# Optimization experiments

Measured on AMD Instinct MI355X. Metric: run time of the kernel, lower is better.

Reference implementation:

```python
import jax, jax.numpy as jnp
import numpy as np

BATCH = 2048
IN_DIM = 512          # group input dim
HID = 1024            # meta_output_dim = dim*2
E = 16                # meta_experts_num = num_experts*2
RANK = 2              # lora_rank
EPS = 1e-5


def setup_inputs() -> dict:
    key = jax.random.key(0)
    ks = jax.random.split(key, 8)
    x = jax.random.normal(ks[0], (BATCH, IN_DIM), jnp.float32)
    gate_states = jax.random.normal(ks[1], (BATCH, IN_DIM), jnp.float32)
    expert_indices = jnp.arange(E, dtype=jnp.int64)
    expert_weights = jax.random.normal(ks[2], (E, IN_DIM, HID), jnp.float32) * 0.02
    expert_biases = jnp.zeros((E, HID), jnp.float32)
    bn_weights = jnp.ones((E, HID), jnp.float32)
    bn_biases = jnp.zeros((E, HID), jnp.float32)
    running_mean = jax.random.normal(ks[3], (E, HID), jnp.float32) * 0.1
    running_var = jnp.abs(jax.random.normal(ks[4], (E, HID), jnp.float32)) * 0.5 + 0.5
    gate_weights = jax.random.normal(ks[5], (IN_DIM, E), jnp.float32) * 0.02
    lora_A = jax.random.normal(ks[6], (IN_DIM, RANK), jnp.float32) * 0.02
    lora_B = jax.random.normal(ks[7], (RANK, IN_DIM), jnp.float32) * 0.02
    return dict(x=x, gate_states=gate_states, expert_indices=expert_indices,
                expert_weights=expert_weights, expert_biases=expert_biases,
                bn_weights=bn_weights, bn_biases=bn_biases,
                running_mean=running_mean, running_var=running_var,
                gate_weights=gate_weights, lora_A=lora_A, lora_B=lora_B)


def reference(x, gate_states, expert_indices, expert_weights, expert_biases,
              bn_weights, bn_biases, running_mean, running_var,
              gate_weights, lora_A, lora_B):
    # LoRA feature gate (lora_gate_forward with sigmoid): x * sigmoid(x A B)
    xg = x * jax.nn.sigmoid((x @ lora_A) @ lora_B)          # [B, D]

    # Expert dispatch: gather selected expert params (home_expert_forward)
    W = expert_weights[expert_indices]                        # [E, D, H]
    b = expert_biases[expert_indices]                         # [E, H]
    h = jnp.einsum('bd,edh->ebh', xg, W) + b[:, None, :]      # [E, B, H]

    # Fused inference BatchNorm + SiLU (fused_batch_norm_silu_forward)
    inv = jax.lax.rsqrt(running_var[expert_indices] + EPS)    # [E, H]
    scale = bn_weights[expert_indices] * inv                  # [E, H]
    shift = bn_biases[expert_indices] - running_mean[expert_indices] * scale
    h = h * scale[:, None, :] + shift[:, None, :]
    h = h * jax.nn.sigmoid(h)                                 # SiLU

    # Softmax gate (gate_weights_forward) and weighted combine
    g = jax.nn.softmax(gate_states @ gate_weights, axis=-1)   # [B, E]
    out = jnp.einsum('ebh,be->bh', h, g)                      # [B, H]
    return out
```

## Files before the change

### kernel.cpp

```cpp
#include <hip/hip_runtime.h>
#include <hip/hip_bf16.h>

#define BATCH 2048
#define IN_DIM 512
#define HID 1024
#define NE 16
#define EPSV 1e-5f

typedef __bf16 bf16x8 __attribute__((ext_vector_type(8)));
typedef float floatx4 __attribute__((ext_vector_type(4)));
typedef unsigned short ushort8 __attribute__((ext_vector_type(8)));

__device__ __forceinline__ unsigned short f2bf(float f) {
  unsigned int u = __builtin_bit_cast(unsigned int, f);
  u += 0x7FFFu + ((u >> 16) & 1u);
  return (unsigned short)(u >> 16);
}

__device__ __forceinline__ int get_expert(const int* __restrict__ idx, int e) {
  bool is64 = (idx[1] == 0) && (idx[3] == 0);
  return is64 ? (int)((const long long*)idx)[e] : idx[e];
}

__device__ __forceinline__ void gld16(void* lds, const void* g) {
  __builtin_amdgcn_global_load_lds(
      (const __attribute__((address_space(1))) void*)g,
      (__attribute__((address_space(3))) void*)lds, 16, 0, 0);
}

__global__ __launch_bounds__(256) void prep_all(
    const int* __restrict__ idx, const float* __restrict__ W,
    unsigned short* __restrict__ WT,
    const float* __restrict__ x, const float* __restrict__ gs,
    const float* __restrict__ gw, const float* __restrict__ lA,
    const float* __restrict__ lB,
    unsigned short* __restrict__ xg, float* __restrict__ g,
    const float* __restrict__ bnw, const float* __restrict__ bnb,
    const float* __restrict__ rmean, const float* __restrict__ rvar,
    const float* __restrict__ ebias,
    float* __restrict__ Ac, float* __restrict__ Cc) {
  int bid = blockIdx.x;
  if (bid < 2048) {
    int e = bid >> 7, kt = (bid >> 4) & 7, ht = bid & 15;
    int ie = get_expert(idx, e);
    int k0 = kt * 64, h0 = ht * 64;
    __shared__ float tile[64][65];
    const float* Wp = W + (size_t)ie * IN_DIM * HID;
#pragma unroll
    for (int i = 0; i < 4; ++i) {
      int id = threadIdx.x + i * 256;
      int k = id >> 4, c = (id & 15) * 4;
      float4 v = *(const float4*)(Wp + (size_t)(k0 + k) * HID + h0 + c);
      tile[k][c] = v.x; tile[k][c + 1] = v.y; tile[k][c + 2] = v.z; tile[k][c + 3] = v.w;
    }
    __syncthreads();
#pragma unroll
    for (int i = 0; i < 2; ++i) {
      int id = threadIdx.x + i * 256;
      int h = id >> 3, kc = (id & 7) * 8;
      ushort8 o;
#pragma unroll
      for (int j = 0; j < 8; ++j) o[j] = f2bf(tile[kc + j][h]);
      *(ushort8*)(WT + ((size_t)e * HID + h0 + h) * IN_DIM + k0 + kc) = o;
    }
  } else if (bid < 2560) {
    int lane = threadIdx.x & 63;
    int b = (bid - 2048) * 4 + (threadIdx.x >> 6);
    const float* xrow = x + (size_t)b * IN_DIM;
    const float* grow = gs + (size_t)b * IN_DIM;
    int d0 = lane * 8;
    float4 xa = *(const float4*)(xrow + d0);
    float4 xb = *(const float4*)(xrow + d0 + 4);
    float xv[8] = {xa.x, xa.y, xa.z, xa.w, xb.x, xb.y, xb.z, xb.w};
    float4 ga = *(const float4*)(grow + d0);
    float4 gb = *(const float4*)(grow + d0 + 4);
    float gv[8] = {ga.x, ga.y, ga.z, ga.w, gb.x, gb.y, gb.z, gb.w};

    float u0 = 0.f, u1 = 0.f;
#pragma unroll
    for (int j = 0; j < 8; ++j) {
      float2 a2 = *(const float2*)(lA + (size_t)(d0 + j) * 2);
      u0 += xv[j] * a2.x;
      u1 += xv[j] * a2.y;
    }
#pragma unroll
    for (int off = 1; off < 64; off <<= 1) {
      u0 += __shfl_xor(u0, off);
      u1 += __shfl_xor(u1, off);
    }
    float ge[16];
#pragma unroll
    for (int e = 0; e < 16; ++e) ge[e] = 0.f;
#pragma unroll
    for (int j = 0; j < 8; ++j) {
      float q = gv[j];
      const float4* gwr = (const float4*)(gw + (size_t)(d0 + j) * NE);
      float4 w0 = gwr[0], w1 = gwr[1], w2 = gwr[2], w3 = gwr[3];
      ge[0] += q * w0.x; ge[1] += q * w0.y; ge[2] += q * w0.z; ge[3] += q * w0.w;
      ge[4] += q * w1.x; ge[5] += q * w1.y; ge[6] += q * w1.z; ge[7] += q * w1.w;
      ge[8] += q * w2.x; ge[9] += q * w2.y; ge[10] += q * w2.z; ge[11] += q * w2.w;
      ge[12] += q * w3.x; ge[13] += q * w3.y; ge[14] += q * w3.z; ge[15] += q * w3.w;
    }
#pragma unroll
    for (int off = 1; off < 64; off <<= 1) {
#pragma unroll
      for (int e = 0; e < 16; ++e) ge[e] += __shfl_xor(ge[e], off);
    }
    float m = ge[0];
#pragma unroll
    for (int e = 1; e < 16; ++e) m = fmaxf(m, ge[e]);
    float p[16], s = 0.f;
#pragma unroll
    for (int e = 0; e < 16; ++e) { p[e] = __expf(ge[e] - m); s += p[e]; }
    float inv = 1.f / s;
    if (lane == 0) {
      float* gout = g + (size_t)b * NE;
#pragma unroll
      for (int e = 0; e < 16; ++e) gout[e] = p[e] * inv;
    }
    ushort8 ov;
#pragma unroll
    for (int j = 0; j < 8; ++j) {
      float t = u0 * lB[d0 + j] + u1 * lB[IN_DIM + d0 + j];
      float sg = __builtin_amdgcn_rcpf(1.f + __expf(-t));
      ov[j] = f2bf(xv[j] * sg);
    }
    *(ushort8*)(xg + (size_t)b * IN_DIM + d0) = ov;
  } else {
    int t = (bid - 2560) * 256 + threadIdx.x;
    int e = t >> 10, h = t & 1023;
    int ie = get_expert(idx, e);
    size_t o = (size_t)ie * HID + h;
    float scale = bnw[o] * rsqrtf(rvar[o] + EPSV);
    Ac[t] = scale;
    Cc[t] = (ebias[o] - rmean[o]) * scale + bnb[o];
  }
}

__global__ __launch_bounds__(256) void zero_out(float* __restrict__ out) {
  int t = blockIdx.x * 256 + threadIdx.x;
  ((float4*)out)[t] = float4{0.f, 0.f, 0.f, 0.f};
}

__global__ __launch_bounds__(256) void reduce4(const float* __restrict__ sws,
                                               float* __restrict__ out) {
  int t = blockIdx.x * 256 + threadIdx.x;
  const float4* s0 = (const float4*)sws;
  const float4* s1 = s0 + (BATCH * HID / 4);
  const float4* s2 = s1 + (BATCH * HID / 4);
  const float4* s3 = s2 + (BATCH * HID / 4);
  float4 a = s0[t], b = s1[t], c = s2[t], d = s3[t];
  ((float4*)out)[t] = float4{a.x + b.x + c.x + d.x, a.y + b.y + c.y + d.y,
                             a.z + b.z + c.z + d.z, a.w + b.w + c.w + d.w};
}

#define BM 128
#define BN 128
#define KS 32
#define EPB 4
#define ESTRIDE ((size_t)HID * IN_DIM)

__global__ __launch_bounds__(256, 2) void moe_main(
    const unsigned short* __restrict__ xg, const unsigned short* __restrict__ WT,
    const float* __restrict__ g, const float* __restrict__ Ac,
    const float* __restrict__ Cc, float* __restrict__ splitws,
    float* __restrict__ out, int use_split) {
  __shared__ __align__(16) unsigned short As[2][2][BM * KS];
  __shared__ __align__(16) unsigned short Bs[2][2][BN * KS];
  __shared__ float gS[BM][EPB];

  int tid = threadIdx.x;
  int lane = tid & 63, w = tid >> 6;
  int wr = w >> 1, wc = w & 1;
  int l15 = lane & 15, quad = lane >> 4;

  int bid = blockIdx.x;
  int p = bid >> 7;
  int rowb = (bid >> 3) & 15, colb = bid & 7;
  int row0 = rowb * BM, col0 = colb * BN;
  int e0 = p * EPB;

  for (int i = tid; i < BM * EPB; i += 256) {
    int r = i >> 2, e = i & 3;
    gS[r][e] = g[(size_t)(row0 + r) * NE + e0 + e];
  }

  int dr = lane >> 2, dk = (lane & 3) * 8;
  const unsigned short* gA = xg + (size_t)(row0 + w * 32 + dr) * IN_DIM + dk;
  const unsigned short* gB0 =
      WT + ((size_t)e0 * HID + col0 + w * 32 + dr) * IN_DIM + dk;

  auto dma = [&](const unsigned short* a, const unsigned short* b, int buf) {
#pragma unroll
    for (int kk = 0; kk < 2; ++kk) {
#pragma unroll
      for (int j = 0; j < 2; ++j) {
        gld16(&As[buf][kk][(w * 32 + j * 16) * KS], a + kk * KS + (size_t)j * 16 * IN_DIM);
        gld16(&Bs[buf][kk][(w * 32 + j * 16) * KS], b + kk * KS + (size_t)j * 16 * IN_DIM);
      }
    }
  };

  floatx4 acc[4][4], oacc[4][4];
#pragma unroll
  for (int rt = 0; rt < 4; ++rt)
#pragma unroll
    for (int ct = 0; ct < 4; ++ct)
#pragma unroll
      for (int r = 0; r < 4; ++r) { acc[rt][ct][r] = 0.f; oacc[rt][ct][r] = 0.f; }

  const unsigned short* gBe = gB0;
  dma(gA, gBe, 0);
  __syncthreads();

  for (int e = 0; e < EPB; ++e) {
    float Acoef[4], Ccoef[4];
#pragma unroll
    for (int ct = 0; ct < 4; ++ct) {
      int colg = col0 + wc * 64 + ct * 16 + l15;
      Acoef[ct] = Ac[(e0 + e) * HID + colg];
      Ccoef[ct] = Cc[(e0 + e) * HID + colg];
    }
#pragma unroll
    for (int s = 0; s < 8; ++s) {
      const int buf = s & 1;
      if (e < EPB - 1 || s < 7) {
        const unsigned short* an = gA + ((s + 1) & 7) * 64;
        const unsigned short* bn = (s < 7) ? (gBe + (s + 1) * 64) : (gBe + ESTRIDE);
        dma(an, bn, buf ^ 1);
      }
#pragma unroll
      for (int kk = 0; kk < 2; ++kk) {
        bf16x8 af[4], bfv[4];
#pragma unroll
        for (int rt = 0; rt < 4; ++rt)
          af[rt] = *(const bf16x8*)&As[buf][kk][(wr * 64 + rt * 16 + l15) * KS + quad * 8];
#pragma unroll
        for (int ct = 0; ct < 4; ++ct)
          bfv[ct] = *(const bf16x8*)&Bs[buf][kk][(wc * 64 + ct * 16 + l15) * KS + quad * 8];
#pragma unroll
        for (int rt = 0; rt < 4; ++rt)
#pragma unroll
          for (int ct = 0; ct < 4; ++ct)
            acc[rt][ct] = __builtin_amdgcn_mfma_f32_16x16x32_bf16(af[rt], bfv[ct], acc[rt][ct], 0, 0, 0);
      }
      if (s == 7) {
#pragma unroll
        for (int ct = 0; ct < 4; ++ct) {
#pragma unroll
          for (int rt = 0; rt < 4; ++rt) {
            int rb = wr * 64 + rt * 16 + quad * 4;
#pragma unroll
            for (int r = 0; r < 4; ++r) {
              float gvw = gS[rb + r][e];
              float z = Acoef[ct] * acc[rt][ct][r] + Ccoef[ct];
              float sg = __builtin_amdgcn_rcpf(1.f + __expf(-z));
              oacc[rt][ct][r] += gvw * z * sg;
              acc[rt][ct][r] = 0.f;
            }
          }
        }
      }
      __syncthreads();
    }
    gBe += ESTRIDE;
  }

  if (use_split) {
    float* sout = splitws + (size_t)p * BATCH * HID;
#pragma unroll
    for (int rt = 0; rt < 4; ++rt)
#pragma unroll
      for (int ct = 0; ct < 4; ++ct)
#pragma unroll
        for (int r = 0; r < 4; ++r)
          sout[(size_t)(row0 + wr * 64 + rt * 16 + quad * 4 + r) * HID +
               col0 + wc * 64 + ct * 16 + l15] = oacc[rt][ct][r];
  } else {
#pragma unroll
    for (int rt = 0; rt < 4; ++rt)
#pragma unroll
      for (int ct = 0; ct < 4; ++ct)
#pragma unroll
        for (int r = 0; r < 4; ++r)
          atomicAdd(&out[(size_t)(row0 + wr * 64 + rt * 16 + quad * 4 + r) * HID +
                         col0 + wc * 64 + ct * 16 + l15], oacc[rt][ct][r]);
  }
}

extern "C" void kernel_launch(void* const* d_in, const int* in_sizes, int n_in,
                              void* d_out, int out_size, void* d_ws, size_t ws_size,
                              hipStream_t stream) {
  const float* x     = (const float*)d_in[0];
  const float* gs    = (const float*)d_in[1];
  const int*   idx   = (const int*)d_in[2];
  const float* W     = (const float*)d_in[3];
  const float* ebias = (const float*)d_in[4];
  const float* bnw   = (const float*)d_in[5];
  const float* bnb   = (const float*)d_in[6];
  const float* rmean = (const float*)d_in[7];
  const float* rvar  = (const float*)d_in[8];
  const float* gw    = (const float*)d_in[9];
  const float* lA    = (const float*)d_in[10];
  const float* lB    = (const float*)d_in[11];
  float* out = (float*)d_out;

  char* ws = (char*)d_ws;
  unsigned short* WT = (unsigned short*)ws;
  unsigned short* xg = (unsigned short*)(ws + 16777216);
  float* g    = (float*)(ws + 18874368);
  float* Acf  = (float*)(ws + 19005440);
  float* Ccf  = (float*)(ws + 19070976);
  float* sws  = (float*)(ws + 19136512);
  int use_split = (ws_size >= 19136512 + 4ull * BATCH * HID * 4) ? 1 : 0;

  prep_all<<<dim3(2624), dim3(256), 0, stream>>>(
      idx, W, WT, x, gs, gw, lA, lB, xg, g, bnw, bnb, rmean, rvar, ebias, Acf, Ccf);
  if (!use_split)
    zero_out<<<dim3(BATCH * HID / 1024), dim3(256), 0, stream>>>(out);
  moe_main<<<dim3((BATCH / BM) * (HID / BN) * (NE / EPB)), dim3(256), 0, stream>>>(
      xg, WT, g, Acf, Ccf, sws, out, use_split);
  if (use_split)
    reduce4<<<dim3(BATCH * HID / 1024), dim3(256), 0, stream>>>(sws, out);
}
```

Measured before the change: 180.6 us.

## Drop split-K workspace reduction, fold output zeroing into prep, hoist LDS fragment loads

Removes the four-way split workspace path and its separate reduce kernel. moe_main now always accumulates into the output with atomicAdd, and zeroing of the output moves into extra blocks of the prep kernel, saving a launch and the extra workspace traffic. The main loop also loads both k-halves of the A/B fragments from LDS before issuing the next DMA, so LDS reads can overlap the prefetch. The cost is contention from four-way float atomics on every output element, a summation order that is no longer deterministic, and higher register pressure from the doubled fragment arrays.

```diff
diff --git a/kernel.cpp b/kernel.cpp
--- a/kernel.cpp
+++ b/kernel.cpp
@@ -38,7 +38,8 @@
     const float* __restrict__ bnw, const float* __restrict__ bnb,
     const float* __restrict__ rmean, const float* __restrict__ rvar,
     const float* __restrict__ ebias,
-    float* __restrict__ Ac, float* __restrict__ Cc) {
+    float* __restrict__ Ac, float* __restrict__ Cc,
+    float* __restrict__ out) {
   int bid = blockIdx.x;
   if (bid < 2048) {
     int e = bid >> 7, kt = (bid >> 4) & 7, ht = bid & 15;
@@ -126,7 +127,7 @@
       ov[j] = f2bf(xv[j] * sg);
     }
     *(ushort8*)(xg + (size_t)b * IN_DIM + d0) = ov;
-  } else {
+  } else if (bid < 2624) {
     int t = (bid - 2560) * 256 + threadIdx.x;
     int e = t >> 10, h = t & 1023;
     int ie = get_expert(idx, e);
@@ -134,24 +135,10 @@
     float scale = bnw[o] * rsqrtf(rvar[o] + EPSV);
     Ac[t] = scale;
     Cc[t] = (ebias[o] - rmean[o]) * scale + bnb[o];
+  } else {
+    int t = (bid - 2624) * 256 + threadIdx.x;
+    ((float4*)out)[t] = float4{0.f, 0.f, 0.f, 0.f};
   }
-}
-
-__global__ __launch_bounds__(256) void zero_out(float* __restrict__ out) {
-  int t = blockIdx.x * 256 + threadIdx.x;
-  ((float4*)out)[t] = float4{0.f, 0.f, 0.f, 0.f};
-}
-
-__global__ __launch_bounds__(256) void reduce4(const float* __restrict__ sws,
-                                               float* __restrict__ out) {
-  int t = blockIdx.x * 256 + threadIdx.x;
-  const float4* s0 = (const float4*)sws;
-  const float4* s1 = s0 + (BATCH * HID / 4);
-  const float4* s2 = s1 + (BATCH * HID / 4);
-  const float4* s3 = s2 + (BATCH * HID / 4);
-  float4 a = s0[t], b = s1[t], c = s2[t], d = s3[t];
-  ((float4*)out)[t] = float4{a.x + b.x + c.x + d.x, a.y + b.y + c.y + d.y,
-                             a.z + b.z + c.z + d.z, a.w + b.w + c.w + d.w};
 }
 
 #define BM 128
@@ -163,8 +150,7 @@
 __global__ __launch_bounds__(256, 2) void moe_main(
     const unsigned short* __restrict__ xg, const unsigned short* __restrict__ WT,
     const float* __restrict__ g, const float* __restrict__ Ac,
-    const float* __restrict__ Cc, float* __restrict__ splitws,
-    float* __restrict__ out, int use_split) {
+    const float* __restrict__ Cc, float* __restrict__ out) {
   __shared__ __align__(16) unsigned short As[2][2][BM * KS];
   __shared__ __align__(16) unsigned short Bs[2][2][BN * KS];
   __shared__ float gS[BM][EPB];
@@ -224,26 +210,28 @@
 #pragma unroll
     for (int s = 0; s < 8; ++s) {
       const int buf = s & 1;
+      bf16x8 af[2][4], bfv[2][4];
+#pragma unroll
+      for (int kk = 0; kk < 2; ++kk) {
+#pragma unroll
+        for (int rt = 0; rt < 4; ++rt)
+          af[kk][rt] = *(const bf16x8*)&As[buf][kk][(wr * 64 + rt * 16 + l15) * KS + quad * 8];
+#pragma unroll
+        for (int ct = 0; ct < 4; ++ct)
+          bfv[kk][ct] = *(const bf16x8*)&Bs[buf][kk][(wc * 64 + ct * 16 + l15) * KS + quad * 8];
+      }
       if (e < EPB - 1 || s < 7) {
         const unsigned short* an = gA + ((s + 1) & 7) * 64;
         const unsigned short* bn = (s < 7) ? (gBe + (s + 1) * 64) : (gBe + ESTRIDE);
         dma(an, bn, buf ^ 1);
       }
 #pragma unroll
-      for (int kk = 0; kk < 2; ++kk) {
-        bf16x8 af[4], bfv[4];
+      for (int kk = 0; kk < 2; ++kk)
 #pragma unroll
         for (int rt = 0; rt < 4; ++rt)
-          af[rt] = *(const bf16x8*)&As[buf][kk][(wr * 64 + rt * 16 + l15) * KS + quad * 8];
-#pragma unroll
-        for (int ct = 0; ct < 4; ++ct)
-          bfv[ct] = *(const bf16x8*)&Bs[buf][kk][(wc * 64 + ct * 16 + l15) * KS + quad * 8];
-#pragma unroll
-        for (int rt = 0; rt < 4; ++rt)
 #pragma unroll
           for (int ct = 0; ct < 4; ++ct)
-            acc[rt][ct] = __builtin_amdgcn_mfma_f32_16x16x32_bf16(af[rt], bfv[ct], acc[rt][ct], 0, 0, 0);
-      }
+            acc[rt][ct] = __builtin_amdgcn_mfma_f32_16x16x32_bf16(af[kk][rt], bfv[kk][ct], acc[rt][ct], 0, 0, 0);
       if (s == 7) {
 #pragma unroll
         for (int ct = 0; ct < 4; ++ct) {
@@ -266,26 +254,14 @@
     gBe += ESTRIDE;
   }
 
-  if (use_split) {
-    float* sout = splitws + (size_t)p * BATCH * HID;
-#pragma unroll
-    for (int rt = 0; rt < 4; ++rt)
-#pragma unroll
-      for (int ct = 0; ct < 4; ++ct)
-#pragma unroll
-        for (int r = 0; r < 4; ++r)
-          sout[(size_t)(row0 + wr * 64 + rt * 16 + quad * 4 + r) * HID +
-               col0 + wc * 64 + ct * 16 + l15] = oacc[rt][ct][r];
-  } else {
-#pragma unroll
-    for (int rt = 0; rt < 4; ++rt)
-#pragma unroll
-      for (int ct = 0; ct < 4; ++ct)
-#pragma unroll
-        for (int r = 0; r < 4; ++r)
-          atomicAdd(&out[(size_t)(row0 + wr * 64 + rt * 16 + quad * 4 + r) * HID +
-                         col0 + wc * 64 + ct * 16 + l15], oacc[rt][ct][r]);
-  }
+#pragma unroll
+  for (int rt = 0; rt < 4; ++rt)
+#pragma unroll
+    for (int ct = 0; ct < 4; ++ct)
+#pragma unroll
+      for (int r = 0; r < 4; ++r)
+        atomicAdd(&out[(size_t)(row0 + wr * 64 + rt * 16 + quad * 4 + r) * HID +
+                       col0 + wc * 64 + ct * 16 + l15], oacc[rt][ct][r]);
 }
 
 extern "C" void kernel_launch(void* const* d_in, const int* in_sizes, int n_in,
@@ -311,15 +287,10 @@
   float* g    = (float*)(ws + 18874368);
   float* Acf  = (float*)(ws + 19005440);
   float* Ccf  = (float*)(ws + 19070976);
-  float* sws  = (float*)(ws + 19136512);
-  int use_split = (ws_size >= 19136512 + 4ull * BATCH * HID * 4) ? 1 : 0;
-
-  prep_all<<<dim3(2624), dim3(256), 0, stream>>>(
-      idx, W, WT, x, gs, gw, lA, lB, xg, g, bnw, bnb, rmean, rvar, ebias, Acf, Ccf);
-  if (!use_split)
-    zero_out<<<dim3(BATCH * HID / 1024), dim3(256), 0, stream>>>(out);
+
+  prep_all<<<dim3(4672), dim3(256), 0, stream>>>(
+      idx, W, WT, x, gs, gw, lA, lB, xg, g, bnw, bnb, rmean, rvar, ebias,
+      Acf, Ccf, out);
   moe_main<<<dim3((BATCH / BM) * (HID / BN) * (NE / EPB)), dim3(256), 0, stream>>>(
-      xg, WT, g, Acf, Ccf, sws, out, use_split);
-  if (use_split)
-    reduce4<<<dim3(BATCH * HID / 1024), dim3(256), 0, stream>>>(sws, out);
-}
+      xg, WT, g, Acf, Ccf, out);
+}
```

Measured after the change: 197.6 us. +9.4%, slower.
